# Performance work log

Measured on AMD Instinct MI355X. Metric: run time of the kernel, lower is better.

Reference implementation:

```python
import jax, jax.numpy as jnp
import numpy as np


def overlap_and_add(frames, step):
    # frames: [B, F, L] -> [B, (F-1)*step + L] via strided scatter-add
    B, F, L = frames.shape
    out_len = (F - 1) * step + L
    idx = (jnp.arange(F)[:, None] * step + jnp.arange(L)[None, :]).reshape(-1)  # [F*L]
    return jnp.zeros((B, out_len), frames.dtype).at[:, idx].add(frames.reshape(B, F * L))


def setup_inputs() -> dict:
    key = jax.random.key(0)
    k1, k2, k3 = jax.random.split(key, 3)
    bs, frame, basis, spk = 16, 4086, 512, 2
    L = 16  # kernel_size_enc
    speech_length = (frame - 1) * (L // 2) + L  # 32696
    inputs = jax.random.normal(k1, (bs, frame, basis), dtype=jnp.float32)
    estmask = jax.random.uniform(k2, (bs, frame, basis, spk), dtype=jnp.float32)
    W = jax.random.normal(k3, (basis, L), dtype=jnp.float32) * 0.05
    return {"inputs": inputs, "estmask": estmask, "W": W,
            "kernel_size_enc": L, "speech_length": speech_length}


def reference(inputs, estmask, W, kernel_size_enc, speech_length):
    bs, frame, basis = inputs.shape
    spk = estmask.shape[-1]
    # mask-weight: [bs, frame, basis, spk]
    x = inputs[..., None] * estmask
    # -> [bs*spk, frame, basis]
    x = jnp.transpose(x, (0, 3, 1, 2)).reshape(bs * spk, frame, basis)
    # dense projection (no bias, no activation): [bs*spk, frame, L]
    x = jnp.einsum('bfc,cl->bfl', x, W)
    # overlap-and-add with frame_step = L // 2
    x = overlap_and_add(x, kernel_size_enc // 2)  # [bs*spk, samples]
    return x.reshape(bs, spk, speech_length)
```

## Files before the change

kernel.cpp:

```cpp
#include <hip/hip_runtime.h>

constexpr int BS = 16, F = 4086, C = 512, SPK = 2, L = 16, STEP = 8;
constexpr int T     = (F - 1) * STEP + L;
constexpr int ROWS  = BS * F;
constexpr int OUT_N = BS * SPK * T;
constexpr int NT    = ROWS / 16;
constexpr int BLOCK = 256, TPB = 4;
constexpr int GRID_M = (NT + TPB - 1) / TPB;
constexpr int WFRAG_DWORDS = 16 * 64 * 4;

typedef _Float16 f16x8 __attribute__((ext_vector_type(8)));
typedef float    f32x4 __attribute__((ext_vector_type(4)));
typedef __fp16   h2    __attribute__((ext_vector_type(2)));

__device__ __forceinline__ unsigned pk(float a, float b) {
    h2 r = __builtin_amdgcn_cvt_pkrtz(a, b);
    return __builtin_bit_cast(unsigned, r);
}

__global__ __launch_bounds__(256) void wstage_kernel(
    const float* __restrict__ W, unsigned* __restrict__ wfrag)
{
    const int t = threadIdx.x;
    const float4* r0 = reinterpret_cast<const float4*>(W + (2 * t) * L);
    const float4* r1 = reinterpret_cast<const float4*>(W + (2 * t + 1) * L);
    const int kt = t >> 4, pr = t & 15;
    const int g  = (pr < 8) ? (pr >> 1) : ((pr - 8) >> 1);
    const int d  = (pr < 8) ? (pr & 1) : (2 + (pr & 1));
#pragma unroll
    for (int q = 0; q < 4; ++q) {
        const float4 a = r0[q], b = r1[q];
        const int c0 = 4 * q;
        wfrag[kt * 256 + (g * 16 + c0 + 0) * 4 + d] = pk(a.x, b.x);
        wfrag[kt * 256 + (g * 16 + c0 + 1) * 4 + d] = pk(a.y, b.y);
        wfrag[kt * 256 + (g * 16 + c0 + 2) * 4 + d] = pk(a.z, b.z);
        wfrag[kt * 256 + (g * 16 + c0 + 3) * 4 + d] = pk(a.w, b.w);
    }
}

struct KtSet { float4 a1, a2, m1, m2, m3, m4; int4 bf; };

__global__ __launch_bounds__(BLOCK, 4) void decoder_mfma_kernel(
    const float* __restrict__ inp,
    const float* __restrict__ mask,
    const unsigned* __restrict__ wfrag,
    float* __restrict__ proj)
{
    const int wave = threadIdx.x >> 6, lane = threadIdx.x & 63;
    const int tile = blockIdx.x * TPB + wave;
    if (tile >= NT) return;

    const int g = lane >> 4, m = lane & 15;
    const int grow = tile * 16 + m;
    const float* ip = inp  + (size_t)grow * C;
    const float* mp = mask + (size_t)grow * (C * SPK);

    auto loadkt = [&](int kt, KtSet& s) {
        const float* i0 = ip + kt * 32 + 4 * g;
        s.a1 = *reinterpret_cast<const float4*>(i0);
        s.a2 = *reinterpret_cast<const float4*>(i0 + 16);
        const float* q0 = mp + kt * 64 + 8 * g;
        s.m1 = *reinterpret_cast<const float4*>(q0);
        s.m2 = *reinterpret_cast<const float4*>(q0 + 4);
        s.m3 = *reinterpret_cast<const float4*>(q0 + 32);
        s.m4 = *reinterpret_cast<const float4*>(q0 + 36);
        s.bf = *reinterpret_cast<const int4*>(wfrag + (kt * 64 + lane) * 4);
    };

    f32x4 acc0 = {0.f, 0.f, 0.f, 0.f}, acc1 = {0.f, 0.f, 0.f, 0.f};
    KtSet cur, nxt;
    loadkt(0, cur);

#pragma unroll
    for (int kt = 0; kt < 16; ++kt) {
        if (kt < 15) loadkt(kt + 1, nxt);

        int4 a0i, a1i;
        a0i.x = pk(cur.a1.x * cur.m1.x, cur.a1.y * cur.m1.z);
        a0i.y = pk(cur.a1.z * cur.m2.x, cur.a1.w * cur.m2.z);
        a0i.z = pk(cur.a2.x * cur.m3.x, cur.a2.y * cur.m3.z);
        a0i.w = pk(cur.a2.z * cur.m4.x, cur.a2.w * cur.m4.z);
        a1i.x = pk(cur.a1.x * cur.m1.y, cur.a1.y * cur.m1.w);
        a1i.y = pk(cur.a1.z * cur.m2.y, cur.a1.w * cur.m2.w);
        a1i.z = pk(cur.a2.x * cur.m3.y, cur.a2.y * cur.m3.w);
        a1i.w = pk(cur.a2.z * cur.m4.y, cur.a2.w * cur.m4.w);

        const f16x8 bf = __builtin_bit_cast(f16x8, cur.bf);
        acc0 = __builtin_amdgcn_mfma_f32_16x16x32_f16(
                   __builtin_bit_cast(f16x8, a0i), bf, acc0, 0, 0, 0);
        acc1 = __builtin_amdgcn_mfma_f32_16x16x32_f16(
                   __builtin_bit_cast(f16x8, a1i), bf, acc1, 0, 0, 0);

        if (kt < 15) cur = nxt;
    }

    const size_t base = (size_t)tile * 16 * 32;
#pragma unroll
    for (int j = 0; j < 4; ++j) {
        const int row = 4 * g + j;
        proj[base + row * 32 + m]      = acc0[j];
        proj[base + row * 32 + 16 + m] = acc1[j];
    }
}

__global__ __launch_bounds__(256) void overlap_add_kernel(
    const float* __restrict__ proj,
    float* __restrict__ out)
{
    const int idx = blockIdx.x * blockDim.x + threadIdx.x;
    if (idx >= OUT_N) return;
    const int b = idx / (SPK * T);
    const int r = idx - b * (SPK * T);
    const int s = r / T;
    const int t = r - s * T;
    const int f0 = t >> 3, l0 = t & 7;
    float acc = 0.f;
    if (t < F * STEP) acc += proj[(size_t)(b * F + f0) * 32 + s * 16 + l0];
    if (t >= STEP)    acc += proj[(size_t)(b * F + f0 - 1) * 32 + s * 16 + 8 + l0];
    out[idx] = acc;
}

extern "C" void kernel_launch(void* const* d_in, const int* in_sizes, int n_in,
                              void* d_out, int out_size, void* d_ws, size_t ws_size,
                              hipStream_t stream) {
    const float* inp  = (const float*)d_in[0];
    const float* mask = (const float*)d_in[1];
    const float* W    = (const float*)d_in[2];
    float* out = (float*)d_out;

    unsigned* wfrag = (unsigned*)d_ws;
    float*    proj  = (float*)d_ws + WFRAG_DWORDS;

    wstage_kernel<<<1, 256, 0, stream>>>(W, wfrag);
    decoder_mfma_kernel<<<GRID_M, BLOCK, 0, stream>>>(inp, mask, wfrag, proj);
    overlap_add_kernel<<<(OUT_N + 255) / 256, 256, 0, stream>>>(proj, out);
}
```

Measured before the change: 93.88 us.

## Stage W fragments in LDS, use contiguous nontemporal loads, vectorize overlap-add

Drops the separate W staging kernel. Each GEMM block now packs W into fp16 MFMA fragments in shared memory, costing one extra barrier and redundant W reads per block. The per-lane K mapping changes so each lane reads contiguous 32B input and 64B mask chunks with nontemporal loads, and the loop is manually double-buffered. The overlap-add kernel now handles four outputs per thread with vector loads and stores, which relies on 16-byte alignment that holds because T and the offsets are multiples of 8.

```diff
diff --git a/kernel.cpp b/kernel.cpp
--- a/kernel.cpp
+++ b/kernel.cpp
@@ -4,10 +4,10 @@
 constexpr int T     = (F - 1) * STEP + L;
 constexpr int ROWS  = BS * F;
 constexpr int OUT_N = BS * SPK * T;
+constexpr int OUT4  = OUT_N / 4;
 constexpr int NT    = ROWS / 16;
 constexpr int BLOCK = 256, TPB = 4;
 constexpr int GRID_M = (NT + TPB - 1) / TPB;
-constexpr int WFRAG_DWORDS = 16 * 64 * 4;
 
 typedef _Float16 f16x8 __attribute__((ext_vector_type(8)));
 typedef float    f32x4 __attribute__((ext_vector_type(4)));
@@ -18,35 +18,34 @@
     return __builtin_bit_cast(unsigned, r);
 }
 
-__global__ __launch_bounds__(256) void wstage_kernel(
-    const float* __restrict__ W, unsigned* __restrict__ wfrag)
-{
-    const int t = threadIdx.x;
-    const float4* r0 = reinterpret_cast<const float4*>(W + (2 * t) * L);
-    const float4* r1 = reinterpret_cast<const float4*>(W + (2 * t + 1) * L);
-    const int kt = t >> 4, pr = t & 15;
-    const int g  = (pr < 8) ? (pr >> 1) : ((pr - 8) >> 1);
-    const int d  = (pr < 8) ? (pr & 1) : (2 + (pr & 1));
-#pragma unroll
-    for (int q = 0; q < 4; ++q) {
-        const float4 a = r0[q], b = r1[q];
-        const int c0 = 4 * q;
-        wfrag[kt * 256 + (g * 16 + c0 + 0) * 4 + d] = pk(a.x, b.x);
-        wfrag[kt * 256 + (g * 16 + c0 + 1) * 4 + d] = pk(a.y, b.y);
-        wfrag[kt * 256 + (g * 16 + c0 + 2) * 4 + d] = pk(a.z, b.z);
-        wfrag[kt * 256 + (g * 16 + c0 + 3) * 4 + d] = pk(a.w, b.w);
-    }
-}
-
-struct KtSet { float4 a1, a2, m1, m2, m3, m4; int4 bf; };
+struct Kt { f32x4 a1, a2, m1, m2, m3, m4; };
 
 __global__ __launch_bounds__(BLOCK, 4) void decoder_mfma_kernel(
     const float* __restrict__ inp,
     const float* __restrict__ mask,
-    const unsigned* __restrict__ wfrag,
+    const float* __restrict__ W,
     float* __restrict__ proj)
 {
-    const int wave = threadIdx.x >> 6, lane = threadIdx.x & 63;
+    __shared__ unsigned wlds[16 * 64 * 4];
+
+    const int tid = threadIdx.x;
+
+    {
+        const int kt = tid >> 4, col = tid & 15;
+#pragma unroll
+        for (int g = 0; g < 4; ++g) {
+#pragma unroll
+            for (int d = 0; d < 4; ++d) {
+                const int r = kt * 32 + 8 * g + 2 * d;
+                const float w0 = W[r * L + col];
+                const float w1 = W[(r + 1) * L + col];
+                wlds[(kt * 64 + g * 16 + col) * 4 + d] = pk(w0, w1);
+            }
+        }
+    }
+    __syncthreads();
+
+    const int wave = tid >> 6, lane = tid & 63;
     const int tile = blockIdx.x * TPB + wave;
     if (tile >= NT) return;
 
@@ -55,44 +54,53 @@
     const float* ip = inp  + (size_t)grow * C;
     const float* mp = mask + (size_t)grow * (C * SPK);
 
-    auto loadkt = [&](int kt, KtSet& s) {
-        const float* i0 = ip + kt * 32 + 4 * g;
-        s.a1 = *reinterpret_cast<const float4*>(i0);
-        s.a2 = *reinterpret_cast<const float4*>(i0 + 16);
-        const float* q0 = mp + kt * 64 + 8 * g;
-        s.m1 = *reinterpret_cast<const float4*>(q0);
-        s.m2 = *reinterpret_cast<const float4*>(q0 + 4);
-        s.m3 = *reinterpret_cast<const float4*>(q0 + 32);
-        s.m4 = *reinterpret_cast<const float4*>(q0 + 36);
-        s.bf = *reinterpret_cast<const int4*>(wfrag + (kt * 64 + lane) * 4);
+    auto loadkt = [&](int kt, Kt& s) {
+        const float* i0 = ip + kt * 32 + 8 * g;
+        s.a1 = __builtin_nontemporal_load(reinterpret_cast<const f32x4*>(i0));
+        s.a2 = __builtin_nontemporal_load(reinterpret_cast<const f32x4*>(i0 + 4));
+        const float* q0 = mp + kt * 64 + 16 * g;
+        s.m1 = __builtin_nontemporal_load(reinterpret_cast<const f32x4*>(q0));
+        s.m2 = __builtin_nontemporal_load(reinterpret_cast<const f32x4*>(q0 + 4));
+        s.m3 = __builtin_nontemporal_load(reinterpret_cast<const f32x4*>(q0 + 8));
+        s.m4 = __builtin_nontemporal_load(reinterpret_cast<const f32x4*>(q0 + 12));
     };
 
     f32x4 acc0 = {0.f, 0.f, 0.f, 0.f}, acc1 = {0.f, 0.f, 0.f, 0.f};
-    KtSet cur, nxt;
-    loadkt(0, cur);
 
-#pragma unroll
-    for (int kt = 0; kt < 16; ++kt) {
-        if (kt < 15) loadkt(kt + 1, nxt);
+    auto compute = [&](int kt, const Kt& s) {
+        int4 a0i, a1i;
+        a0i.x = pk(s.a1[0] * s.m1[0], s.a1[1] * s.m1[2]);
+        a0i.y = pk(s.a1[2] * s.m2[0], s.a1[3] * s.m2[2]);
+        a0i.z = pk(s.a2[0] * s.m3[0], s.a2[1] * s.m3[2]);
+        a0i.w = pk(s.a2[2] * s.m4[0], s.a2[3] * s.m4[2]);
+        a1i.x = pk(s.a1[0] * s.m1[1], s.a1[1] * s.m1[3]);
+        a1i.y = pk(s.a1[2] * s.m2[1], s.a1[3] * s.m2[3]);
+        a1i.z = pk(s.a2[0] * s.m3[1], s.a2[1] * s.m3[3]);
+        a1i.w = pk(s.a2[2] * s.m4[1], s.a2[3] * s.m4[3]);
+        const int4 bw = *reinterpret_cast<const int4*>(&wlds[(kt * 64 + lane) * 4]);
+        const f16x8 bf = __builtin_bit_cast(f16x8, bw);
+        acc0 = __builtin_amdgcn_mfma_f32_16x16x32_f16(__builtin_bit_cast(f16x8, a0i), bf, acc0, 0, 0, 0);
+        acc1 = __builtin_amdgcn_mfma_f32_16x16x32_f16(__builtin_bit_cast(f16x8, a1i), bf, acc1, 0, 0, 0);
+    };
 
-        int4 a0i, a1i;
-        a0i.x = pk(cur.a1.x * cur.m1.x, cur.a1.y * cur.m1.z);
-        a0i.y = pk(cur.a1.z * cur.m2.x, cur.a1.w * cur.m2.z);
-        a0i.z = pk(cur.a2.x * cur.m3.x, cur.a2.y * cur.m3.z);
-        a0i.w = pk(cur.a2.z * cur.m4.x, cur.a2.w * cur.m4.z);
-        a1i.x = pk(cur.a1.x * cur.m1.y, cur.a1.y * cur.m1.w);
-        a1i.y = pk(cur.a1.z * cur.m2.y, cur.a1.w * cur.m2.w);
-        a1i.z = pk(cur.a2.x * cur.m3.y, cur.a2.y * cur.m3.w);
-        a1i.w = pk(cur.a2.z * cur.m4.y, cur.a2.w * cur.m4.w);
-
-        const f16x8 bf = __builtin_bit_cast(f16x8, cur.bf);
-        acc0 = __builtin_amdgcn_mfma_f32_16x16x32_f16(
-                   __builtin_bit_cast(f16x8, a0i), bf, acc0, 0, 0, 0);
-        acc1 = __builtin_amdgcn_mfma_f32_16x16x32_f16(
-                   __builtin_bit_cast(f16x8, a1i), bf, acc1, 0, 0, 0);
-
-        if (kt < 15) cur = nxt;
-    }
+    Kt A, B;
+    loadkt(0, A); loadkt(1, B);
+    compute(0,  A); loadkt(2,  A);
+    compute(1,  B); loadkt(3,  B);
+    compute(2,  A); loadkt(4,  A);
+    compute(3,  B); loadkt(5,  B);
+    compute(4,  A); loadkt(6,  A);
+    compute(5,  B); loadkt(7,  B);
+    compute(6,  A); loadkt(8,  A);
+    compute(7,  B); loadkt(9,  B);
+    compute(8,  A); loadkt(10, A);
+    compute(9,  B); loadkt(11, B);
+    compute(10, A); loadkt(12, A);
+    compute(11, B); loadkt(13, B);
+    compute(12, A); loadkt(14, A);
+    compute(13, B); loadkt(15, B);
+    compute(14, A);
+    compute(15, B);
 
     const size_t base = (size_t)tile * 16 * 32;
 #pragma unroll
@@ -103,21 +111,26 @@
     }
 }
 
-__global__ __launch_bounds__(256) void overlap_add_kernel(
+__global__ __launch_bounds__(256) void overlap_add4_kernel(
     const float* __restrict__ proj,
     float* __restrict__ out)
 {
-    const int idx = blockIdx.x * blockDim.x + threadIdx.x;
-    if (idx >= OUT_N) return;
-    const int b = idx / (SPK * T);
-    const int r = idx - b * (SPK * T);
+    const int i4 = blockIdx.x * blockDim.x + threadIdx.x;
+    if (i4 >= OUT4) return;
+    const int t4 = i4 * 4;
+    const int b = t4 / (SPK * T);
+    const int r = t4 - b * (SPK * T);
     const int s = r / T;
     const int t = r - s * T;
     const int f0 = t >> 3, l0 = t & 7;
-    float acc = 0.f;
-    if (t < F * STEP) acc += proj[(size_t)(b * F + f0) * 32 + s * 16 + l0];
-    if (t >= STEP)    acc += proj[(size_t)(b * F + f0 - 1) * 32 + s * 16 + 8 + l0];
-    out[idx] = acc;
+    f32x4 acc = {0.f, 0.f, 0.f, 0.f};
+    if (t < F * STEP)
+        acc = *reinterpret_cast<const f32x4*>(&proj[(size_t)(b * F + f0) * 32 + s * 16 + l0]);
+    if (t >= STEP) {
+        const f32x4 p = *reinterpret_cast<const f32x4*>(&proj[(size_t)(b * F + f0 - 1) * 32 + s * 16 + 8 + l0]);
+        acc += p;
+    }
+    *reinterpret_cast<f32x4*>(&out[t4]) = acc;
 }
 
 extern "C" void kernel_launch(void* const* d_in, const int* in_sizes, int n_in,
@@ -128,10 +141,8 @@
     const float* W    = (const float*)d_in[2];
     float* out = (float*)d_out;
 
-    unsigned* wfrag = (unsigned*)d_ws;
-    float*    proj  = (float*)d_ws + WFRAG_DWORDS;
+    float* proj = (float*)d_ws;
 
-    wstage_kernel<<<1, 256, 0, stream>>>(W, wfrag);
-    decoder_mfma_kernel<<<GRID_M, BLOCK, 0, stream>>>(inp, mask, wfrag, proj);
-    overlap_add_kernel<<<(OUT_N + 255) / 256, 256, 0, stream>>>(proj, out);
+    decoder_mfma_kernel<<<GRID_M, BLOCK, 0, stream>>>(inp, mask, W, proj);
+    overlap_add4_kernel<<<(OUT4 + 255) / 256, 256, 0, stream>>>(proj, out);
 }
```

Result: slower. 128.8 us (+37.1%).
